# Performance work log

Measured on AMD Instinct MI355X. Metric: run time of the kernel, lower is better.

Reference implementation:

```python
import jax, jax.numpy as jnp
import numpy as np

N_NODES = 100000
N_EDGES = 6400000
NUM_FEATURES = 50
HID1, HID2 = 30, 25


def setup_inputs() -> dict:
    key = jax.random.key(0)
    k_x, k_e, k_w1, k_b1, k_w2, k_b2 = jax.random.split(key, 6)
    x = jax.random.normal(k_x, (N_NODES, NUM_FEATURES), dtype=jnp.float32)
    edge_index = jax.random.randint(k_e, (2, N_EDGES), 0, N_NODES, dtype=jnp.int64)
    # Glorot-style init like PyG GCNConv
    W1 = jax.random.normal(k_w1, (NUM_FEATURES, HID1), dtype=jnp.float32) * (1.0 / np.sqrt(NUM_FEATURES))
    b1 = jnp.zeros((HID1,), dtype=jnp.float32)
    W2 = jax.random.normal(k_w2, (HID1, HID2), dtype=jnp.float32) * (1.0 / np.sqrt(HID1))
    b2 = jnp.zeros((HID2,), dtype=jnp.float32)
    return {"x": x, "edge_index": edge_index, "W1": W1, "b1": b1, "W2": W2, "b2": b2}


def reference(x, edge_index, W1, b1, W2, b2):
    """Two-layer GCN (PyG GCNConv semantics, eval mode so dropout is identity).

    GCNConv: out = D^{-1/2} (A + I) D^{-1/2} (x @ W) + b,
    with messages flowing source (row) -> target (col).
    """
    N = x.shape[0]
    loop = jnp.arange(N, dtype=edge_index.dtype)
    src = jnp.concatenate([edge_index[0], loop])  # [E+N]
    dst = jnp.concatenate([edge_index[1], loop])  # [E+N]
    # degree (incl. self-loops) at target nodes; >= 1 so rsqrt is safe
    deg = jax.ops.segment_sum(jnp.ones_like(dst, dtype=x.dtype), dst, num_segments=N)
    dinv = jax.lax.rsqrt(deg)
    norm = dinv[src] * dinv[dst]  # [E+N]

    def gcn_layer(h, W, b):
        h = h @ W                                   # [N, F_out] small GEMM
        msgs = norm[:, None] * h[src]               # gather + scale
        agg = jax.ops.segment_sum(msgs, dst, num_segments=N)  # scatter-add
        return agg + b

    h = jax.nn.relu(gcn_layer(x, W1, b1))
    # F.dropout with training=False is identity (eval-mode reference)
    return gcn_layer(h, W2, b2)
```

## Files before the change

### kernel.cpp

```cpp
#include <hip/hip_runtime.h>
#include <hip/hip_bf16.h>
#include <hip/hip_fp16.h>

#define NN 100000
#define NE 6400000
#define F_IN 50
#define H1 30
#define H2 25

#define BSZ 128
#define NB 782
#define NBLK 256
#define CHUNK 25000
#define CAP 12160
#define M_TOT (NB * NBLK)
#define SBLK ((M_TOT + 1023) / 1024)

__global__ __launch_bounds__(1024) void k_hist(const int* __restrict__ dst,
                                               int* __restrict__ cntT) {
    __shared__ int h[NB];
    for (int i = threadIdx.x; i < NB; i += 1024) h[i] = 0;
    __syncthreads();
    int base = blockIdx.x * CHUNK;
    for (int i = threadIdx.x; i < CHUNK; i += 1024)
        atomicAdd(&h[dst[base + i] >> 7], 1);
    __syncthreads();
    for (int i = threadIdx.x; i < NB; i += 1024)
        cntT[i * NBLK + blockIdx.x] = h[i];
}

__global__ __launch_bounds__(1024) void k_scan1(int* __restrict__ buf,
                                                int* __restrict__ bsum) {
    __shared__ int tmp[1024];
    int b = blockIdx.x, t = threadIdx.x;
    int i = b * 1024 + t;
    int v = (i < M_TOT) ? buf[i] : 0;
    tmp[t] = v;
    __syncthreads();
    for (int off = 1; off < 1024; off <<= 1) {
        int u = (t >= off) ? tmp[t - off] : 0;
        __syncthreads();
        tmp[t] += u;
        __syncthreads();
    }
    if (i < M_TOT) buf[i] = tmp[t] - v;
    if (t == 1023) bsum[b] = tmp[1023];
}

__global__ __launch_bounds__(256) void k_scan2(int* __restrict__ bsum) {
    __shared__ int tmp[256];
    int t = threadIdx.x;
    int v = (t < SBLK) ? bsum[t] : 0;
    tmp[t] = v;
    __syncthreads();
    for (int off = 1; off < 256; off <<= 1) {
        int u = (t >= off) ? tmp[t - off] : 0;
        __syncthreads();
        tmp[t] += u;
        __syncthreads();
    }
    if (t < SBLK) bsum[t] = tmp[t] - v;
}

__global__ __launch_bounds__(1024) void k_scan3(int* __restrict__ buf,
                                                const int* __restrict__ bsum) {
    int i = blockIdx.x * 1024 + threadIdx.x;
    if (i < M_TOT) buf[i] += bsum[blockIdx.x];
}

__global__ __launch_bounds__(1024) void k_place(const int* __restrict__ src,
                                                const int* __restrict__ dst,
                                                const int* __restrict__ offT,
                                                int* __restrict__ ebuf) {
    __shared__ int cur[NB];
    for (int i = threadIdx.x; i < NB; i += 1024)
        cur[i] = offT[i * NBLK + blockIdx.x];
    __syncthreads();
    int base = blockIdx.x * CHUNK;
    for (int i = threadIdx.x; i < CHUNK; i += 1024) {
        int d = dst[base + i];
        int s = src[base + i];
        int b = d >> 7;
        int p = atomicAdd(&cur[b], 1);
        ebuf[p] = (s << 7) | (d & 127);
    }
}

__global__ __launch_bounds__(256) void k_bsort(int* __restrict__ ebuf,
                                               const int* __restrict__ offT,
                                               int* __restrict__ rowptr) {
    __shared__ int keys[CAP];
    __shared__ int cnt[BSZ];
    __shared__ int loc[BSZ];
    int b = blockIdx.x;
    int beg = offT[b * NBLK];
    int end = (b == NB - 1) ? NE : offT[(b + 1) * NBLK];
    int m = end - beg; if (m > CAP) m = CAP;
    int t = threadIdx.x;
    if (t < BSZ) cnt[t] = 0;
    __syncthreads();
    for (int i = t; i < m; i += 256) {
        int k = ebuf[beg + i];
        keys[i] = k;
        atomicAdd(&cnt[k & 127], 1);
    }
    __syncthreads();
    if (t < BSZ) loc[t] = cnt[t];
    __syncthreads();
    for (int off = 1; off < BSZ; off <<= 1) {
        int v = (t < BSZ && t >= off) ? loc[t - off] : 0;
        __syncthreads();
        if (t < BSZ) loc[t] += v;
        __syncthreads();
    }
    int nbase = b * BSZ;
    int nloc = NN - nbase; if (nloc > BSZ) nloc = BSZ;
    if (t < nloc) {
        int excl = loc[t] - cnt[t];
        rowptr[nbase + t] = beg + excl;
        if (t == nloc - 1) rowptr[nbase + nloc] = beg + loc[t];
    }
    __syncthreads();
    if (t < BSZ) cnt[t] = beg + loc[t] - cnt[t];
    __syncthreads();
    for (int i = t; i < m; i += 256) {
        int k = keys[i];
        int p = atomicAdd(&cnt[k & 127], 1);
        ebuf[p] = k >> 7;
    }
}

__global__ __launch_bounds__(256) void k_gemm1(const float* __restrict__ x,
                                               const float* __restrict__ W1,
                                               const int* __restrict__ rowptr,
                                               __half* __restrict__ h1ph) {
    __shared__ float Ws[F_IN * H1];
    for (int i = threadIdx.x; i < F_IN * H1; i += 256) Ws[i] = W1[i];
    __syncthreads();
    int n = blockIdx.x * 256 + threadIdx.x;
    if (n >= NN) return;
    float dn = rsqrtf((float)(rowptr[n + 1] - rowptr[n] + 1));
    float xr[F_IN];
#pragma unroll
    for (int k = 0; k < F_IN; ++k) xr[k] = x[n * F_IN + k];
    float o[32];
#pragma unroll
    for (int j = 0; j < H1; ++j) {
        float a = 0.f;
#pragma unroll
        for (int k = 0; k < F_IN; ++k) a = fmaf(xr[k], Ws[k * H1 + j], a);
        o[j] = dn * a;
    }
    o[30] = 0.f; o[31] = 0.f;
    union { unsigned int u[16]; uint4 q[4]; } pk;
#pragma unroll
    for (int j = 0; j < 16; ++j) {
        __half2 hh = __halves2half2(__float2half(o[2 * j]), __float2half(o[2 * j + 1]));
        pk.u[j] = *reinterpret_cast<unsigned int*>(&hh);
    }
    uint4* d4 = (uint4*)&h1ph[n * 32];
#pragma unroll
    for (int q = 0; q < 4; ++q) d4[q] = pk.q[q];
}

__global__ __launch_bounds__(256) void k_agg1(const int* __restrict__ ebuf,
                                              const int* __restrict__ rowptr,
                                              const __half* __restrict__ h1ph,
                                              const float* __restrict__ W2,
                                              const float* __restrict__ b1,
                                              __half* __restrict__ t2sh) {
    __shared__ float W2s[H1 * H2];
    __shared__ float b1s[H1];
    __shared__ float a_lds[16][32];
    for (int i = threadIdx.x; i < H1 * H2; i += 256) W2s[i] = W2[i];
    if (threadIdx.x < H1) b1s[threadIdx.x] = b1[threadIdx.x];
    __syncthreads();

    int g = threadIdx.x >> 4;
    int l = threadIdx.x & 15;
    int n = blockIdx.x * 16 + g;

    int beg = 0, end = 0;
    if (n < NN) { beg = rowptr[n]; end = rowptr[n + 1]; }
    int m = end - beg;
    int nfull = m & ~15;
    float ax = 0.f, ay = 0.f;
    for (int base = beg; base < beg + nfull; base += 16) {
        int sv = ebuf[base + l];
#pragma unroll
        for (int jb = 0; jb < 16; jb += 8) {
            int ss[8];
            __half2 v[8];
#pragma unroll
            for (int u = 0; u < 8; ++u) ss[u] = __shfl(sv, jb + u, 16);
#pragma unroll
            for (int u = 0; u < 8; ++u)
                v[u] = *(const __half2*)&h1ph[ss[u] * 32 + 2 * l];
#pragma unroll
            for (int u = 0; u < 8; ++u) {
                float2 f2 = __half22float2(v[u]);
                ax += f2.x; ay += f2.y;
            }
        }
    }
    int rem = m - nfull;
    if (rem) {
        int sv = (l < rem) ? ebuf[beg + nfull + l] : 0;
        for (int i = 0; i < rem; ++i) {
            int s = __shfl(sv, i, 16);
            float2 f2 = __half22float2(*(const __half2*)&h1ph[s * 32 + 2 * l]);
            ax += f2.x; ay += f2.y;
        }
    }
    if (n < NN) {
        float dn = rsqrtf((float)(m + 1));
        float2 self = __half22float2(*(const __half2*)&h1ph[n * 32 + 2 * l]);
        int j0 = 2 * l, j1 = 2 * l + 1;
        float v0 = (j0 < H1) ? fmaxf(dn * (ax + self.x) + b1s[j0], 0.f) : 0.f;
        float v1 = (j1 < H1) ? fmaxf(dn * (ay + self.y) + b1s[j1], 0.f) : 0.f;
        a_lds[g][j0] = v0;
        a_lds[g][j1] = v1;
    }
    __syncthreads();
    if (n < NN) {
        float dn = rsqrtf((float)(m + 1));
        int j0 = 2 * l, j1 = 2 * l + 1;
        float t0 = 0.f, t1 = 0.f;
#pragma unroll
        for (int k = 0; k < H1; ++k) {
            float a = a_lds[g][k];
            if (j0 < H2) t0 = fmaf(a, W2s[k * H2 + j0], t0);
            if (j1 < H2) t1 = fmaf(a, W2s[k * H2 + j1], t1);
        }
        t0 = (j0 < H2) ? dn * t0 : 0.f;
        t1 = (j1 < H2) ? dn * t1 : 0.f;
        __half2 hh = __halves2half2(__float2half(t0), __float2half(t1));
        *(__half2*)&t2sh[n * 32 + 2 * l] = hh;
    }
}

__global__ __launch_bounds__(256) void k_agg2(const int* __restrict__ ebuf,
                                              const int* __restrict__ rowptr,
                                              const __half* __restrict__ t2sh,
                                              const float* __restrict__ b2,
                                              float* __restrict__ out) {
    __shared__ float b2s[H2];
    if (threadIdx.x < H2) b2s[threadIdx.x] = b2[threadIdx.x];
    __syncthreads();
    int g = threadIdx.x >> 4;
    int l = threadIdx.x & 15;
    int n = blockIdx.x * 16 + g;
    if (n >= NN) return;
    int beg = rowptr[n], end = rowptr[n + 1];
    int m = end - beg;
    float dn = rsqrtf((float)(m + 1));
    float ax = 0.f, ay = 0.f;
    int nfull = m & ~15;
    for (int base = beg; base < beg + nfull; base += 16) {
        int sv = ebuf[base + l];
#pragma unroll
        for (int jb = 0; jb < 16; jb += 8) {
            int ss[8];
            __half2 v[8];
#pragma unroll
            for (int u = 0; u < 8; ++u) ss[u] = __shfl(sv, jb + u, 16);
#pragma unroll
            for (int u = 0; u < 8; ++u)
                v[u] = *(const __half2*)&t2sh[ss[u] * 32 + 2 * l];
#pragma unroll
            for (int u = 0; u < 8; ++u) {
                float2 f2 = __half22float2(v[u]);
                ax += f2.x; ay += f2.y;
            }
        }
    }
    int rem = m - nfull;
    if (rem) {
        int sv = (l < rem) ? ebuf[beg + nfull + l] : 0;
        for (int i = 0; i < rem; ++i) {
            int s = __shfl(sv, i, 16);
            float2 f2 = __half22float2(*(const __half2*)&t2sh[s * 32 + 2 * l]);
            ax += f2.x; ay += f2.y;
        }
    }
    float2 self = __half22float2(*(const __half2*)&t2sh[n * 32 + 2 * l]);
    int j0 = 2 * l, j1 = 2 * l + 1;
    if (j0 < H2) out[n * H2 + j0] = dn * (ax + self.x) + b2s[j0];
    if (j1 < H2) out[n * H2 + j1] = dn * (ay + self.y) + b2s[j1];
}

extern "C" void kernel_launch(void* const* d_in, const int* in_sizes, int n_in,
                              void* d_out, int out_size, void* d_ws, size_t ws_size,
                              hipStream_t stream) {
    const float* x   = (const float*)d_in[0];
    const int*   ei  = (const int*)d_in[1];
    const float* W1  = (const float*)d_in[2];
    const float* b1  = (const float*)d_in[3];
    const float* W2  = (const float*)d_in[4];
    const float* b2  = (const float*)d_in[5];
    float*       out = (float*)d_out;

    const int* src = ei;
    const int* dst = ei + NE;

    char* ws = (char*)d_ws;
    int*    rowptr = (int*)   (ws + 0);
    int*    offT   = (int*)   (ws + 400128);
    int*    bsum   = (int*)   (ws + 1201024);
    __half* h1ph   = (__half*)(ws + 1201920);
    __half* t2sh   = (__half*)(ws + 7601920);
    int*    ebuf   = (int*)   (ws + 14001920);

    k_hist <<<NBLK, 1024, 0, stream>>>(dst, offT);
    k_scan1<<<SBLK, 1024, 0, stream>>>(offT, bsum);
    k_scan2<<<1, 256, 0, stream>>>(bsum);
    k_scan3<<<SBLK, 1024, 0, stream>>>(offT, bsum);
    k_place<<<NBLK, 1024, 0, stream>>>(src, dst, offT, ebuf);
    k_bsort<<<NB, 256, 0, stream>>>(ebuf, offT, rowptr);
    k_gemm1<<<(NN + 255) / 256, 256, 0, stream>>>(x, W1, rowptr, h1ph);
    k_agg1 <<<(NN + 15) / 16, 256, 0, stream>>>(ebuf, rowptr, h1ph, W2, b1, t2sh);
    k_agg2 <<<(NN + 15) / 16, 256, 0, stream>>>(ebuf, rowptr, t2sh, b2, out);
}
```

Before: 295.9 us.

## Split feature tables into halves for cache-resident gathers; locally sort edges in place

The aggregation kernels now gather from 16-half-wide (32-byte) feature tables split into low and high halves, each processed in its own pass, so each gathered table is about 3.2 MB and has a better chance of staying in cache. The W2 matmul, previously fused into the first aggregation, moves to a separate k_gemm2 kernel. k_place now buckets each chunk's edges in shared memory with a local scan before writing them out, so global writes are contiguous rather than scattered. In exchange the edge list and rowptr are read twice per layer, and there are extra launches plus an intermediate activation buffer round-trip.

```diff
diff --git a/kernel.cpp b/kernel.cpp
--- a/kernel.cpp
+++ b/kernel.cpp
@@ -12,6 +12,7 @@
 #define NB 782
 #define NBLK 256
 #define CHUNK 25000
+#define EPT ((CHUNK + 1023) / 1024)
 #define CAP 12160
 #define M_TOT (NB * NBLK)
 #define SBLK ((M_TOT + 1023) / 1024)
@@ -72,17 +73,56 @@
                                                 const int* __restrict__ dst,
                                                 const int* __restrict__ offT,
                                                 int* __restrict__ ebuf) {
-    __shared__ int cur[NB];
-    for (int i = threadIdx.x; i < NB; i += 1024)
-        cur[i] = offT[i * NBLK + blockIdx.x];
-    __syncthreads();
+    __shared__ int keys[CHUNK];
+    __shared__ int cnt[NB];
+    __shared__ int lstart[NB];
+    __shared__ int gbase[NB];
+    __shared__ int scanT[1024];
+    int t = threadIdx.x;
     int base = blockIdx.x * CHUNK;
-    for (int i = threadIdx.x; i < CHUNK; i += 1024) {
-        int d = dst[base + i];
-        int s = src[base + i];
-        int b = d >> 7;
-        int p = atomicAdd(&cur[b], 1);
-        ebuf[p] = (s << 7) | (d & 127);
+    for (int i = t; i < NB; i += 1024) {
+        cnt[i] = 0;
+        gbase[i] = offT[i * NBLK + blockIdx.x];
+    }
+    __syncthreads();
+    int sreg[EPT], breg[EPT];
+#pragma unroll
+    for (int k = 0; k < EPT; ++k) {
+        int idx = k * 1024 + t;
+        if (idx < CHUNK) {
+            int d = dst[base + idx];
+            int s = src[base + idx];
+            breg[k] = d >> 7;
+            sreg[k] = (s << 7) | (d & 127);
+            atomicAdd(&cnt[breg[k]], 1);
+        }
+    }
+    __syncthreads();
+    int v = (t < NB) ? cnt[t] : 0;
+    scanT[t] = v;
+    __syncthreads();
+    for (int off = 1; off < 1024; off <<= 1) {
+        int u = (t >= off) ? scanT[t - off] : 0;
+        __syncthreads();
+        scanT[t] += u;
+        __syncthreads();
+    }
+    if (t < NB) { int e = scanT[t] - v; lstart[t] = e; cnt[t] = e; }
+    __syncthreads();
+#pragma unroll
+    for (int k = 0; k < EPT; ++k) {
+        int idx = k * 1024 + t;
+        if (idx < CHUNK) {
+            int p = atomicAdd(&cnt[breg[k]], 1);
+            keys[p] = sreg[k];
+        }
+    }
+    __syncthreads();
+    int wv = t >> 6, ln = t & 63;
+    for (int b = wv; b < NB; b += 16) {
+        int s0 = lstart[b], e0 = cnt[b], gb = gbase[b];
+        for (int off = ln; off < e0 - s0; off += 64)
+            ebuf[gb + off] = keys[s0 + off];
     }
 }
 
@@ -133,7 +173,8 @@
 __global__ __launch_bounds__(256) void k_gemm1(const float* __restrict__ x,
                                                const float* __restrict__ W1,
                                                const int* __restrict__ rowptr,
-                                               __half* __restrict__ h1ph) {
+                                               __half* __restrict__ h1lo,
+                                               __half* __restrict__ h1hi) {
     __shared__ float Ws[F_IN * H1];
     for (int i = threadIdx.x; i < F_IN * H1; i += 256) Ws[i] = W1[i];
     __syncthreads();
@@ -158,135 +199,142 @@
         __half2 hh = __halves2half2(__float2half(o[2 * j]), __float2half(o[2 * j + 1]));
         pk.u[j] = *reinterpret_cast<unsigned int*>(&hh);
     }
-    uint4* d4 = (uint4*)&h1ph[n * 32];
-#pragma unroll
-    for (int q = 0; q < 4; ++q) d4[q] = pk.q[q];
-}
-
-__global__ __launch_bounds__(256) void k_agg1(const int* __restrict__ ebuf,
-                                              const int* __restrict__ rowptr,
-                                              const __half* __restrict__ h1ph,
-                                              const float* __restrict__ W2,
-                                              const float* __restrict__ b1,
-                                              __half* __restrict__ t2sh) {
-    __shared__ float W2s[H1 * H2];
-    __shared__ float b1s[H1];
-    __shared__ float a_lds[16][32];
-    for (int i = threadIdx.x; i < H1 * H2; i += 256) W2s[i] = W2[i];
-    if (threadIdx.x < H1) b1s[threadIdx.x] = b1[threadIdx.x];
-    __syncthreads();
-
-    int g = threadIdx.x >> 4;
-    int l = threadIdx.x & 15;
-    int n = blockIdx.x * 16 + g;
-
-    int beg = 0, end = 0;
-    if (n < NN) { beg = rowptr[n]; end = rowptr[n + 1]; }
+    uint4* lo = (uint4*)&h1lo[n * 16];
+    uint4* hi = (uint4*)&h1hi[n * 16];
+    lo[0] = pk.q[0]; lo[1] = pk.q[1];
+    hi[0] = pk.q[2]; hi[1] = pk.q[3];
+}
+
+__global__ __launch_bounds__(256) void k_aggh1(const int* __restrict__ ebuf,
+                                               const int* __restrict__ rowptr,
+                                               const __half* __restrict__ tab,
+                                               const float* __restrict__ b1,
+                                               int fbase,
+                                               __half* __restrict__ a_buf) {
+    __shared__ float bb[16];
+    if (threadIdx.x < 16) {
+        int j = fbase + threadIdx.x;
+        bb[threadIdx.x] = (j < H1) ? b1[j] : 0.f;
+    }
+    __syncthreads();
+    int g = threadIdx.x >> 3;
+    int l = threadIdx.x & 7;
+    int n = blockIdx.x * 32 + g;
+    int beg = rowptr[n], end = rowptr[n + 1];
     int m = end - beg;
-    int nfull = m & ~15;
+    int nfull = m & ~7;
     float ax = 0.f, ay = 0.f;
-    for (int base = beg; base < beg + nfull; base += 16) {
+    for (int base = beg; base < beg + nfull; base += 8) {
         int sv = ebuf[base + l];
-#pragma unroll
-        for (int jb = 0; jb < 16; jb += 8) {
-            int ss[8];
-            __half2 v[8];
-#pragma unroll
-            for (int u = 0; u < 8; ++u) ss[u] = __shfl(sv, jb + u, 16);
-#pragma unroll
-            for (int u = 0; u < 8; ++u)
-                v[u] = *(const __half2*)&h1ph[ss[u] * 32 + 2 * l];
-#pragma unroll
-            for (int u = 0; u < 8; ++u) {
-                float2 f2 = __half22float2(v[u]);
-                ax += f2.x; ay += f2.y;
-            }
-        }
+        int ss[8]; __half2 vv[8];
+#pragma unroll
+        for (int u = 0; u < 8; ++u) ss[u] = __shfl(sv, u, 8);
+#pragma unroll
+        for (int u = 0; u < 8; ++u) vv[u] = *(const __half2*)&tab[ss[u] * 16 + 2 * l];
+#pragma unroll
+        for (int u = 0; u < 8; ++u) { float2 f = __half22float2(vv[u]); ax += f.x; ay += f.y; }
     }
     int rem = m - nfull;
     if (rem) {
         int sv = (l < rem) ? ebuf[beg + nfull + l] : 0;
         for (int i = 0; i < rem; ++i) {
-            int s = __shfl(sv, i, 16);
-            float2 f2 = __half22float2(*(const __half2*)&h1ph[s * 32 + 2 * l]);
-            ax += f2.x; ay += f2.y;
+            int s = __shfl(sv, i, 8);
+            float2 f = __half22float2(*(const __half2*)&tab[s * 16 + 2 * l]);
+            ax += f.x; ay += f.y;
         }
     }
-    if (n < NN) {
-        float dn = rsqrtf((float)(m + 1));
-        float2 self = __half22float2(*(const __half2*)&h1ph[n * 32 + 2 * l]);
-        int j0 = 2 * l, j1 = 2 * l + 1;
-        float v0 = (j0 < H1) ? fmaxf(dn * (ax + self.x) + b1s[j0], 0.f) : 0.f;
-        float v1 = (j1 < H1) ? fmaxf(dn * (ay + self.y) + b1s[j1], 0.f) : 0.f;
-        a_lds[g][j0] = v0;
-        a_lds[g][j1] = v1;
-    }
-    __syncthreads();
-    if (n < NN) {
-        float dn = rsqrtf((float)(m + 1));
-        int j0 = 2 * l, j1 = 2 * l + 1;
-        float t0 = 0.f, t1 = 0.f;
-#pragma unroll
-        for (int k = 0; k < H1; ++k) {
-            float a = a_lds[g][k];
-            if (j0 < H2) t0 = fmaf(a, W2s[k * H2 + j0], t0);
-            if (j1 < H2) t1 = fmaf(a, W2s[k * H2 + j1], t1);
-        }
-        t0 = (j0 < H2) ? dn * t0 : 0.f;
-        t1 = (j1 < H2) ? dn * t1 : 0.f;
-        __half2 hh = __halves2half2(__float2half(t0), __float2half(t1));
-        *(__half2*)&t2sh[n * 32 + 2 * l] = hh;
-    }
-}
-
-__global__ __launch_bounds__(256) void k_agg2(const int* __restrict__ ebuf,
-                                              const int* __restrict__ rowptr,
-                                              const __half* __restrict__ t2sh,
-                                              const float* __restrict__ b2,
-                                              float* __restrict__ out) {
-    __shared__ float b2s[H2];
-    if (threadIdx.x < H2) b2s[threadIdx.x] = b2[threadIdx.x];
-    __syncthreads();
-    int g = threadIdx.x >> 4;
-    int l = threadIdx.x & 15;
-    int n = blockIdx.x * 16 + g;
+    float dn = rsqrtf((float)(m + 1));
+    float2 self = __half22float2(*(const __half2*)&tab[n * 16 + 2 * l]);
+    int j0 = fbase + 2 * l, j1 = j0 + 1;
+    float v0 = (j0 < H1) ? fmaxf(dn * (ax + self.x) + bb[2 * l], 0.f) : 0.f;
+    float v1 = (j1 < H1) ? fmaxf(dn * (ay + self.y) + bb[2 * l + 1], 0.f) : 0.f;
+    *(__half2*)&a_buf[n * 32 + fbase + 2 * l] =
+        __halves2half2(__float2half(v0), __float2half(v1));
+}
+
+__global__ __launch_bounds__(256) void k_gemm2(const __half* __restrict__ a_buf,
+                                               const float* __restrict__ W2,
+                                               const int* __restrict__ rowptr,
+                                               __half* __restrict__ t2lo,
+                                               __half* __restrict__ t2hi) {
+    __shared__ float Ws[H1 * H2];
+    for (int i = threadIdx.x; i < H1 * H2; i += 256) Ws[i] = W2[i];
+    __syncthreads();
+    int n = blockIdx.x * 256 + threadIdx.x;
     if (n >= NN) return;
+    float a[H1];
+    const __half2* ar = (const __half2*)&a_buf[n * 32];
+#pragma unroll
+    for (int k = 0; k < 15; ++k) {
+        float2 f = __half22float2(ar[k]);
+        a[2 * k] = f.x; a[2 * k + 1] = f.y;
+    }
+    float dn = rsqrtf((float)(rowptr[n + 1] - rowptr[n] + 1));
+    float o[32];
+#pragma unroll
+    for (int j = 0; j < H2; ++j) {
+        float acc = 0.f;
+#pragma unroll
+        for (int k = 0; k < H1; ++k) acc = fmaf(a[k], Ws[k * H2 + j], acc);
+        o[j] = dn * acc;
+    }
+#pragma unroll
+    for (int j = H2; j < 32; ++j) o[j] = 0.f;
+    union { unsigned int u[16]; uint4 q[4]; } pk;
+#pragma unroll
+    for (int j = 0; j < 16; ++j) {
+        __half2 hh = __halves2half2(__float2half(o[2 * j]), __float2half(o[2 * j + 1]));
+        pk.u[j] = *reinterpret_cast<unsigned int*>(&hh);
+    }
+    uint4* lo = (uint4*)&t2lo[n * 16];
+    uint4* hi = (uint4*)&t2hi[n * 16];
+    lo[0] = pk.q[0]; lo[1] = pk.q[1];
+    hi[0] = pk.q[2]; hi[1] = pk.q[3];
+}
+
+__global__ __launch_bounds__(256) void k_aggh2(const int* __restrict__ ebuf,
+                                               const int* __restrict__ rowptr,
+                                               const __half* __restrict__ tab,
+                                               const float* __restrict__ b2,
+                                               int fbase,
+                                               float* __restrict__ out) {
+    __shared__ float bb[16];
+    if (threadIdx.x < 16) {
+        int j = fbase + threadIdx.x;
+        bb[threadIdx.x] = (j < H2) ? b2[j] : 0.f;
+    }
+    __syncthreads();
+    int g = threadIdx.x >> 3;
+    int l = threadIdx.x & 7;
+    int n = blockIdx.x * 32 + g;
     int beg = rowptr[n], end = rowptr[n + 1];
     int m = end - beg;
-    float dn = rsqrtf((float)(m + 1));
+    int nfull = m & ~7;
     float ax = 0.f, ay = 0.f;
-    int nfull = m & ~15;
-    for (int base = beg; base < beg + nfull; base += 16) {
+    for (int base = beg; base < beg + nfull; base += 8) {
         int sv = ebuf[base + l];
-#pragma unroll
-        for (int jb = 0; jb < 16; jb += 8) {
-            int ss[8];
-            __half2 v[8];
-#pragma unroll
-            for (int u = 0; u < 8; ++u) ss[u] = __shfl(sv, jb + u, 16);
-#pragma unroll
-            for (int u = 0; u < 8; ++u)
-                v[u] = *(const __half2*)&t2sh[ss[u] * 32 + 2 * l];
-#pragma unroll
-            for (int u = 0; u < 8; ++u) {
-                float2 f2 = __half22float2(v[u]);
-                ax += f2.x; ay += f2.y;
-            }
-        }
+        int ss[8]; __half2 vv[8];
+#pragma unroll
+        for (int u = 0; u < 8; ++u) ss[u] = __shfl(sv, u, 8);
+#pragma unroll
+        for (int u = 0; u < 8; ++u) vv[u] = *(const __half2*)&tab[ss[u] * 16 + 2 * l];
+#pragma unroll
+        for (int u = 0; u < 8; ++u) { float2 f = __half22float2(vv[u]); ax += f.x; ay += f.y; }
     }
     int rem = m - nfull;
     if (rem) {
         int sv = (l < rem) ? ebuf[beg + nfull + l] : 0;
         for (int i = 0; i < rem; ++i) {
-            int s = __shfl(sv, i, 16);
-            float2 f2 = __half22float2(*(const __half2*)&t2sh[s * 32 + 2 * l]);
-            ax += f2.x; ay += f2.y;
+            int s = __shfl(sv, i, 8);
+            float2 f = __half22float2(*(const __half2*)&tab[s * 16 + 2 * l]);
+            ax += f.x; ay += f.y;
         }
     }
-    float2 self = __half22float2(*(const __half2*)&t2sh[n * 32 + 2 * l]);
-    int j0 = 2 * l, j1 = 2 * l + 1;
-    if (j0 < H2) out[n * H2 + j0] = dn * (ax + self.x) + b2s[j0];
-    if (j1 < H2) out[n * H2 + j1] = dn * (ay + self.y) + b2s[j1];
+    float dn = rsqrtf((float)(m + 1));
+    float2 self = __half22float2(*(const __half2*)&tab[n * 16 + 2 * l]);
+    int j0 = fbase + 2 * l, j1 = j0 + 1;
+    if (j0 < H2) out[n * H2 + j0] = dn * (ax + self.x) + bb[2 * l];
+    if (j1 < H2) out[n * H2 + j1] = dn * (ay + self.y) + bb[2 * l + 1];
 }
 
 extern "C" void kernel_launch(void* const* d_in, const int* in_sizes, int n_in,
@@ -307,9 +355,12 @@
     int*    rowptr = (int*)   (ws + 0);
     int*    offT   = (int*)   (ws + 400128);
     int*    bsum   = (int*)   (ws + 1201024);
-    __half* h1ph   = (__half*)(ws + 1201920);
-    __half* t2sh   = (__half*)(ws + 7601920);
-    int*    ebuf   = (int*)   (ws + 14001920);
+    __half* h1lo   = (__half*)(ws + 1201920);
+    __half* h1hi   = (__half*)(ws + 4401920);
+    __half* abuf   = (__half*)(ws + 7601920);
+    __half* t2lo   = (__half*)(ws + 14001920);
+    __half* t2hi   = (__half*)(ws + 17201920);
+    int*    ebuf   = (int*)   (ws + 20401920);
 
     k_hist <<<NBLK, 1024, 0, stream>>>(dst, offT);
     k_scan1<<<SBLK, 1024, 0, stream>>>(offT, bsum);
@@ -317,7 +368,10 @@
     k_scan3<<<SBLK, 1024, 0, stream>>>(offT, bsum);
     k_place<<<NBLK, 1024, 0, stream>>>(src, dst, offT, ebuf);
     k_bsort<<<NB, 256, 0, stream>>>(ebuf, offT, rowptr);
-    k_gemm1<<<(NN + 255) / 256, 256, 0, stream>>>(x, W1, rowptr, h1ph);
-    k_agg1 <<<(NN + 15) / 16, 256, 0, stream>>>(ebuf, rowptr, h1ph, W2, b1, t2sh);
-    k_agg2 <<<(NN + 15) / 16, 256, 0, stream>>>(ebuf, rowptr, t2sh, b2, out);
-}
+    k_gemm1<<<(NN + 255) / 256, 256, 0, stream>>>(x, W1, rowptr, h1lo, h1hi);
+    k_aggh1<<<NN / 32, 256, 0, stream>>>(ebuf, rowptr, h1lo, b1, 0,  abuf);
+    k_aggh1<<<NN / 32, 256, 0, stream>>>(ebuf, rowptr, h1hi, b1, 16, abuf);
+    k_gemm2<<<(NN + 255) / 256, 256, 0, stream>>>(abuf, W2, rowptr, t2lo, t2hi);
+    k_aggh2<<<NN / 32, 256, 0, stream>>>(ebuf, rowptr, t2lo, b2, 0,  out);
+    k_aggh2<<<NN / 32, 256, 0, stream>>>(ebuf, rowptr, t2hi, b2, 16, out);
+}
```

New measurement: 307.9 us. +4.1%, slower.
